# Performance work log

Hardware: AMD Instinct MI355X
Metric: run time of the kernel (lower is better)

Reference implementation:

```python
import jax, jax.numpy as jnp
import numpy as np

NUM_HEAD = 32
NUM_KV_HEAD = 8
HEAD_DIM = 128
EMBED_DIM = 4096
GROUP = NUM_HEAD // NUM_KV_HEAD + 2  # 6: 4 q slots + 1 k + 1 v
TOKENS = 64


def setup_inputs() -> dict:
    key = jax.random.key(0)
    k1, k2, k3 = jax.random.split(key, 3)
    inp = jax.random.normal(k1, (TOKENS, EMBED_DIM), dtype=jnp.float32)
    # fused GQA weight layout from load_parameter: [embed_dim, num_kv_head, group, head_dim]
    weight = jax.random.normal(k2, (EMBED_DIM, NUM_KV_HEAD, GROUP, HEAD_DIM), dtype=jnp.float32) * 0.02
    bias = jax.random.normal(k3, (NUM_KV_HEAD, GROUP, HEAD_DIM), dtype=jnp.float32) * 0.02
    return {"input": inp, "weight": weight, "bias": bias}


def reference(input, weight, bias):
    # fused grouped QKV GEMM (mm_qkv_group_out):
    # out[t, kv, g, d] = sum_e input[t, e] * weight[e, kv, g, d] + bias[kv, g, d]
    out = jnp.einsum('te,ekgd->tkgd', input, weight) + bias
    T = input.shape[0]
    q = out[:, :, : GROUP - 2, :].reshape(T, NUM_HEAD * HEAD_DIM)
    k = out[:, :, GROUP - 2, :].reshape(T, NUM_KV_HEAD * HEAD_DIM)
    v = out[:, :, GROUP - 1, :].reshape(T, NUM_KV_HEAD * HEAD_DIM)
    return (q, k, v)
```

## Files before the change

kernel.cpp:

```cpp
#include <hip/hip_runtime.h>


#define N_COLS 6144
#define K_DIM  4096
#define Q_SZ   (64 * 4096)
#define K_OFF  Q_SZ
#define V_OFF  (Q_SZ + 64 * 1024)
#define OUT_ELEMS 393216
#define NT     48
#define KSPLIT 16
#define BK     32
#define TILES  8

typedef __bf16 bf16x8 __attribute__((ext_vector_type(8)));
typedef float  f32x4  __attribute__((ext_vector_type(4)));

__device__ __forceinline__ int out_index(int t, int n) {
    const int kv = n / 768;
    const int g  = (n >> 7) % 6;
    const int d  = n & 127;
    if (g < 4)  return t * 4096 + kv * 512 + g * 128 + d;
    if (g == 4) return K_OFF + t * 1024 + kv * 128 + d;
    return V_OFF + t * 1024 + kv * 128 + d;
}

#define GLDS(gp, lp) __builtin_amdgcn_global_load_lds(                        \
    (const __attribute__((address_space(1))) void*)(gp),                      \
    (__attribute__((address_space(3))) void*)(lp), 16, 0, 0)

#define VWAIT4() asm volatile("s_waitcnt vmcnt(4)" ::: "memory")

__global__ __launch_bounds__(256, 3)
void qkv_gemm(const float* __restrict__ in, const float* __restrict__ w,
              float* __restrict__ part) {
    __shared__ float Ws[2][BK * 128];

    const int tid  = threadIdx.x;
    const int nt   = blockIdx.x % NT;
    const int kq   = blockIdx.x / NT;
    const int n0   = nt * 128;
    const int k0   = kq * (BK * TILES);
    const int wid  = tid >> 6;
    const int lane = tid & 63;
    const int l15  = lane & 15;
    const int kblk = lane >> 4;

    f32x4 acc[2][4];
    #pragma unroll
    for (int a = 0; a < 2; ++a)
        #pragma unroll
        for (int b = 0; b < 4; ++b) acc[a][b] = (f32x4){0.f, 0.f, 0.f, 0.f};

    float4 aloA[4], ahiA[4], aloB[4], ahiB[4];

    auto STAGE = [&](int s, int buf) {
        const int kc = k0 + s * BK;
        const float* wr = w + (size_t)kc * N_COLS + n0;
        #pragma unroll
        for (int r = 0; r < 4; ++r) {
            const int u = r * 256 + tid;
            const int c = (u & 31) ^ (((u >> 8) & 3) << 2);
            GLDS(wr + (size_t)(u >> 5) * N_COLS + c * 4, &Ws[buf][u * 4]);
        }
    };

    auto LOADA = [&](int s, float4 (&alo)[4], float4 (&ahi)[4]) {
        const int kc = k0 + s * BK;
        #pragma unroll
        for (int mi = 0; mi < 4; ++mi) {
            const float* ap = in + (size_t)(mi * 16 + l15) * K_DIM + kc + kblk * 8;
            alo[mi] = *(const float4*)ap;
            ahi[mi] = *(const float4*)(ap + 4);
        }
    };

    auto BODY = [&](const float4 (&alo)[4], const float4 (&ahi)[4], int buf) {
        bf16x8 av[4];
        #pragma unroll
        for (int mi = 0; mi < 4; ++mi) {
            av[mi][0] = (__bf16)alo[mi].x; av[mi][1] = (__bf16)alo[mi].y;
            av[mi][2] = (__bf16)alo[mi].z; av[mi][3] = (__bf16)alo[mi].w;
            av[mi][4] = (__bf16)ahi[mi].x; av[mi][5] = (__bf16)ahi[mi].y;
            av[mi][6] = (__bf16)ahi[mi].z; av[mi][7] = (__bf16)ahi[mi].w;
        }
        #pragma unroll
        for (int nfi = 0; nfi < 2; ++nfi) {
            const int nb   = (wid * 2 + nfi) * 16 + l15;
            const int base = kblk * 1024 + (nb ^ (kblk << 4));
            bf16x8 bv;
            #pragma unroll
            for (int j = 0; j < 8; ++j)
                bv[j] = (__bf16)Ws[buf][base + j * 128];
            #pragma unroll
            for (int mi = 0; mi < 4; ++mi)
                acc[nfi][mi] = __builtin_amdgcn_mfma_f32_16x16x32_bf16(
                    av[mi], bv, acc[nfi][mi], 0, 0, 0);
        }
    };

    STAGE(0, 0);
    LOADA(0, aloA, ahiA);

    #pragma unroll
    for (int s = 0; s < TILES; ++s) {
        if (s + 1 < TILES) STAGE(s + 1, (s + 1) & 1);
        VWAIT4();
        __builtin_amdgcn_s_barrier();
        if ((s & 1) == 0) {
            if (s + 1 < TILES) LOADA(s + 1, aloB, ahiB);
            BODY(aloA, ahiA, 0);
        } else {
            if (s + 1 < TILES) LOADA(s + 1, aloA, ahiA);
            BODY(aloB, ahiB, 1);
        }
        __builtin_amdgcn_s_barrier();
    }

    float* pb = part + (size_t)kq * OUT_ELEMS;
    #pragma unroll
    for (int nfi = 0; nfi < 2; ++nfi) {
        const int n = n0 + (wid * 2 + nfi) * 16 + l15;
        #pragma unroll
        for (int mi = 0; mi < 4; ++mi) {
            #pragma unroll
            for (int r = 0; r < 4; ++r) {
                const int t = mi * 16 + kblk * 4 + r;
                pb[(size_t)t * N_COLS + n] = acc[nfi][mi][r];
            }
        }
    }
}

__global__ __launch_bounds__(256)
void qkv_reduce(const float* __restrict__ part, const float* __restrict__ bias,
                float* __restrict__ out) {
    const int i = (blockIdx.x * 256 + threadIdx.x) << 2;
    const int t = i / N_COLS;
    const int n = i - t * N_COLS;
    f32x4 s = *(const f32x4*)(bias + n);
    #pragma unroll
    for (int kq = 0; kq < KSPLIT; ++kq)
        s += *(const f32x4*)(part + (size_t)kq * OUT_ELEMS + i);
    *(f32x4*)(out + out_index(t, n)) = s;
}

extern "C" void kernel_launch(void* const* d_in, const int* in_sizes, int n_in,
                              void* d_out, int out_size, void* d_ws, size_t ws_size,
                              hipStream_t stream) {
    const float* in   = (const float*)d_in[0];
    const float* w    = (const float*)d_in[1];
    const float* bias = (const float*)d_in[2];
    float* out  = (float*)d_out;
    float* part = (float*)d_ws;

    qkv_gemm<<<NT * KSPLIT, 256, 0, stream>>>(in, w, part);
    qkv_reduce<<<OUT_ELEMS / 1024, 256, 0, stream>>>(part, bias, out);
}
```

Baseline: 162.7 us.

## Stage weight tiles through registers with two-deep prefetch instead of direct-to-LDS loads

```diff
diff --git a/kernel.cpp b/kernel.cpp
--- a/kernel.cpp
+++ b/kernel.cpp
@@ -24,12 +24,6 @@
     return V_OFF + t * 1024 + kv * 128 + d;
 }
 
-#define GLDS(gp, lp) __builtin_amdgcn_global_load_lds(                        \
-    (const __attribute__((address_space(1))) void*)(gp),                      \
-    (__attribute__((address_space(3))) void*)(lp), 16, 0, 0)
-
-#define VWAIT4() asm volatile("s_waitcnt vmcnt(4)" ::: "memory")
-
 __global__ __launch_bounds__(256, 3)
 void qkv_gemm(const float* __restrict__ in, const float* __restrict__ w,
               float* __restrict__ part) {
@@ -45,26 +39,33 @@
     const int l15  = lane & 15;
     const int kblk = lane >> 4;
 
+    const int t5 = tid >> 5;
+    const int c  = tid & 31;
+
     f32x4 acc[2][4];
     #pragma unroll
     for (int a = 0; a < 2; ++a)
         #pragma unroll
         for (int b = 0; b < 4; ++b) acc[a][b] = (f32x4){0.f, 0.f, 0.f, 0.f};
 
-    float4 aloA[4], ahiA[4], aloB[4], ahiB[4];
+    f32x4 wreg[2][4];
+    float4 alo[4], ahi[4];
 
-    auto STAGE = [&](int s, int buf) {
-        const int kc = k0 + s * BK;
-        const float* wr = w + (size_t)kc * N_COLS + n0;
+    const float* wbase = w + (size_t)k0 * N_COLS + n0 + c * 4;
+
+    auto WLOAD = [&](int s, int set) {
+        const float* p = wbase + (size_t)s * BK * N_COLS;
         #pragma unroll
-        for (int r = 0; r < 4; ++r) {
-            const int u = r * 256 + tid;
-            const int c = (u & 31) ^ (((u >> 8) & 3) << 2);
-            GLDS(wr + (size_t)(u >> 5) * N_COLS + c * 4, &Ws[buf][u * 4]);
-        }
+        for (int r = 0; r < 4; ++r)
+            wreg[set][r] = *(const f32x4*)(p + (size_t)(r * 8 + t5) * N_COLS);
     };
-
-    auto LOADA = [&](int s, float4 (&alo)[4], float4 (&ahi)[4]) {
+    auto DSWRITE = [&](int set, int buf) {
+        #pragma unroll
+        for (int r = 0; r < 4; ++r)
+            *(f32x4*)&Ws[buf][(r * 8 + t5) * 128 + 4 * (c ^ (r << 2))] =
+                wreg[set][r];
+    };
+    auto ALOAD = [&](int s) {
         const int kc = k0 + s * BK;
         #pragma unroll
         for (int mi = 0; mi < 4; ++mi) {
@@ -74,7 +75,15 @@
         }
     };
 
-    auto BODY = [&](const float4 (&alo)[4], const float4 (&ahi)[4], int buf) {
+    WLOAD(0, 0);
+    ALOAD(0);
+    WLOAD(1, 1);
+    DSWRITE(0, 0);
+    asm volatile("s_waitcnt lgkmcnt(0)" ::: "memory");
+    __builtin_amdgcn_s_barrier();
+
+    #pragma unroll
+    for (int s = 0; s < TILES; ++s) {
         bf16x8 av[4];
         #pragma unroll
         for (int mi = 0; mi < 4; ++mi) {
@@ -83,6 +92,10 @@
             av[mi][4] = (__bf16)ahi[mi].x; av[mi][5] = (__bf16)ahi[mi].y;
             av[mi][6] = (__bf16)ahi[mi].z; av[mi][7] = (__bf16)ahi[mi].w;
         }
+
+        if (s + 2 < TILES) WLOAD(s + 2, s & 1);
+        if (s + 1 < TILES) ALOAD(s + 1);
+
         #pragma unroll
         for (int nfi = 0; nfi < 2; ++nfi) {
             const int nb   = (wid * 2 + nfi) * 16 + l15;
@@ -90,30 +103,18 @@
             bf16x8 bv;
             #pragma unroll
             for (int j = 0; j < 8; ++j)
-                bv[j] = (__bf16)Ws[buf][base + j * 128];
+                bv[j] = (__bf16)Ws[s & 1][base + j * 128];
             #pragma unroll
             for (int mi = 0; mi < 4; ++mi)
                 acc[nfi][mi] = __builtin_amdgcn_mfma_f32_16x16x32_bf16(
                     av[mi], bv, acc[nfi][mi], 0, 0, 0);
         }
-    };
 
-    STAGE(0, 0);
-    LOADA(0, aloA, ahiA);
-
-    #pragma unroll
-    for (int s = 0; s < TILES; ++s) {
-        if (s + 1 < TILES) STAGE(s + 1, (s + 1) & 1);
-        VWAIT4();
-        __builtin_amdgcn_s_barrier();
-        if ((s & 1) == 0) {
-            if (s + 1 < TILES) LOADA(s + 1, aloB, ahiB);
-            BODY(aloA, ahiA, 0);
-        } else {
-            if (s + 1 < TILES) LOADA(s + 1, aloA, ahiA);
-            BODY(aloB, ahiB, 1);
+        if (s + 1 < TILES) {
+            DSWRITE((s + 1) & 1, (s + 1) & 1);
+            asm volatile("s_waitcnt lgkmcnt(0)" ::: "memory");
+            __builtin_amdgcn_s_barrier();
         }
-        __builtin_amdgcn_s_barrier();
     }
 
     float* pb = part + (size_t)kq * OUT_ELEMS;
```

Result: no change. 164.8 us (+1.3%).
